# Performance work log

Hardware: AMD Instinct MI355X
Metric: run time of the kernel (lower is better)

The kernel has to match this reference:

```python
import jax, jax.numpy as jnp
import numpy as np

NUM_HEADS = 16
MASKED_BIAS = -10000.0


def setup_inputs() -> dict:
    key = jax.random.key(0)
    k1, k2, k3 = jax.random.split(key, 3)
    B, S, D = 4, 2048, 1024
    return {
        "hidden_states": jax.random.normal(k1, (B, S, D), dtype=jnp.float32),
        "attention_mask": jnp.ones((B, S), dtype=jnp.float32),
        "w_attn": jax.random.normal(k2, (D, 3 * D), dtype=jnp.float32) * 0.02,
        "b_attn": jax.random.normal(k3, (3 * D,), dtype=jnp.float32) * 0.1,
    }


def reference(hidden_states, attention_mask, w_attn, b_attn):
    B, S, D = hidden_states.shape
    H = NUM_HEADS
    Dh = D // H
    # Conv1D: x @ W + b  -> [B, S, 3D]
    qkv = hidden_states @ w_attn + b_attn
    q, k, v = jnp.split(qkv, 3, axis=-1)

    def split_heads(t):  # [B,S,D] -> [B,H,S,Dh]
        return t.reshape(B, S, H, Dh).transpose(0, 2, 1, 3)

    q, k, v = split_heads(q), split_heads(k), split_heads(v)
    present = jnp.stack([k, v], axis=0)  # concat_key_value

    # process_mask: (1 - mask) * -10000, broadcast [B,1,1,S]
    add_mask = (1.0 - attention_mask)[:, None, None, :] * MASKED_BIAS

    qk = jnp.einsum("bhqd,bhkd->bhqk", q, k)
    norm_qk = qk * (1.0 / float(Dh) ** 0.5)
    causal = jnp.tril(jnp.ones((S, S), dtype=bool))[None, None]
    attn_weights = jnp.where(causal, norm_qk, jnp.asarray(MASKED_BIAS, norm_qk.dtype))
    attn_weights = attn_weights + add_mask
    probs = jax.nn.softmax(attn_weights, axis=-1)
    attn_output = jnp.einsum("bhqk,bhkd->bhqd", probs, v)
    # merge heads -> [B,S,D]
    attn_output = attn_output.transpose(0, 2, 1, 3).reshape(B, S, D)
    return attn_output, present
```

## Files before the change

### kernel.cpp

```cpp
#include <hip/hip_runtime.h>
#include <stdint.h>


#define B_SZ    4
#define S_LEN   2048
#define D_MODEL 1024
#define N3      3072
#define H_NUM   16
#define DH      64
#define M_TOT   8192

typedef __attribute__((ext_vector_type(8))) short short8;
typedef __attribute__((ext_vector_type(4))) short bf16x4;
typedef __attribute__((ext_vector_type(4))) float f32x4;

#define LOG2E      1.4426950408889634f
#define SCL2E      0.18033688011112042f
#define MASKB2     (-14426.9504f)

__device__ __forceinline__ unsigned short f2b(float f) {
  union { float f; unsigned int u; } x;
  x.f = f;
  unsigned int u = x.u;
  u += 0x7fffu + ((u >> 16) & 1u);
  return (unsigned short)(u >> 16);
}

__device__ __forceinline__ unsigned int cvt_pk_bf16(float lo, float hi) {
  unsigned int r;
  asm("v_cvt_pk_bf16_f32 %0, %1, %2" : "=v"(r) : "v"(lo), "v"(hi));
  return r;
}

__device__ __forceinline__ float exp2_fast(float x) {
#if __has_builtin(__builtin_amdgcn_exp2f)
  return __builtin_amdgcn_exp2f(x);
#else
  return __expf(x * 0.6931471805599453f);
#endif
}

__device__ __forceinline__ f32x4 mfma16(bf16x4 a, bf16x4 b, f32x4 c) {
#if __has_builtin(__builtin_amdgcn_mfma_f32_16x16x16bf16_1k)
  return __builtin_amdgcn_mfma_f32_16x16x16bf16_1k(a, b, c, 0, 0, 0);
#else
  asm("v_mfma_f32_16x16x16_bf16 %0, %1, %2, %0" : "+v"(c) : "v"(a), "v"(b));
  return c;
#endif
}

__device__ __forceinline__ void async16(const void* g, void* l) {
  __builtin_amdgcn_global_load_lds((const __attribute__((address_space(1))) void*)g,
                                   (__attribute__((address_space(3))) void*)l,
                                   16, 0, 0);
}

__global__ void k_convert_x(const float* __restrict__ X, unsigned short* __restrict__ Xb) {
  const int i = (blockIdx.x * 256 + threadIdx.x) * 4;
  const float4 v = *(const float4*)(X + i);
  ushort4 o;
  o.x = f2b(v.x); o.y = f2b(v.y); o.z = f2b(v.z); o.w = f2b(v.w);
  *(ushort4*)(Xb + i) = o;
}

__global__ void k_wt(const float* __restrict__ W, unsigned short* __restrict__ Wt) {
  __shared__ float tile[32][33];
  const int n0 = blockIdx.x * 32, k0 = blockIdx.y * 32;
  const int tx = threadIdx.x, ty = threadIdx.y;
  for (int i = 0; i < 32; i += 8)
    tile[ty + i][tx] = W[(size_t)(k0 + ty + i) * N3 + n0 + tx];
  __syncthreads();
  for (int i = 0; i < 32; i += 8)
    Wt[(size_t)(n0 + ty + i) * D_MODEL + k0 + tx] = f2b(tile[tx][ty + i]);
}

__global__ __launch_bounds__(256) void k_gemm_qkv(
    const unsigned short* __restrict__ Xb, const unsigned short* __restrict__ Wt,
    const float* __restrict__ bias,
    unsigned short* __restrict__ Qb, unsigned short* __restrict__ Kb,
    float* __restrict__ presK, float* __restrict__ presV) {
  __shared__ __align__(16) unsigned short As[128 * 32];
  __shared__ __align__(16) unsigned short Bs[128 * 32];
  const int t = threadIdx.x;
  const int lane = t & 63, wave = t >> 6;
  const int g = lane >> 4, c = lane & 15;
  const int m0 = blockIdx.y * 128, n0 = blockIdx.x * 128;
  const int wm = (wave >> 1) * 64, wn = (wave & 1) * 64;

  const f32x4 zero = {0.f, 0.f, 0.f, 0.f};
  f32x4 acc[4][4];
  for (int i = 0; i < 4; ++i)
    for (int j = 0; j < 4; ++j) acc[i][j] = zero;

  const int row_a = t >> 2;
  const int col_a = (t & 3) * 8;
  const unsigned short* gA = Xb + (size_t)(m0 + row_a) * D_MODEL + col_a;
  const unsigned short* gB = Wt + (size_t)(n0 + row_a) * D_MODEL + col_a;
  const int wbase = wave * 1024;

  for (int k0 = 0; k0 < D_MODEL; k0 += 32) {
    __syncthreads();
    async16(gA + k0,                (char*)As + wbase);
    async16(gA + k0 + 64 * D_MODEL, (char*)As + 4096 + wbase);
    async16(gB + k0,                (char*)Bs + wbase);
    async16(gB + k0 + 64 * D_MODEL, (char*)Bs + 4096 + wbase);
    __syncthreads();

    short8 af[4], bf[4];
    for (int mi = 0; mi < 4; ++mi)
      af[mi] = *(const short8*)(As + (wm + mi * 16 + c) * 32 + g * 8);
    for (int ni = 0; ni < 4; ++ni)
      bf[ni] = *(const short8*)(Bs + (wn + ni * 16 + c) * 32 + g * 8);
    for (int mi = 0; mi < 4; ++mi)
      for (int ni = 0; ni < 4; ++ni)
        acc[mi][ni] = __builtin_amdgcn_mfma_f32_16x16x32_bf16(af[mi], bf[ni], acc[mi][ni], 0, 0, 0);
  }

  for (int ni = 0; ni < 4; ++ni) {
    const int n = n0 + wn + ni * 16 + c;
    const float bv = bias[n];
    const int sec = n >> 10;
    const int d = n & 1023;
    const int h = d >> 6, dh = d & 63;
    for (int mi = 0; mi < 4; ++mi) {
      for (int r = 0; r < 4; ++r) {
        const int m = m0 + wm + mi * 16 + g * 4 + r;
        const int b = m >> 11, s = m & 2047;
        const float val = acc[mi][ni][r] + bv;
        const size_t hidx = ((size_t)((b * H_NUM + h) * S_LEN + s)) * DH + dh;
        if (sec == 0) {
          Qb[hidx] = f2b(val);
        } else if (sec == 1) {
          presK[hidx] = val;
          Kb[hidx] = f2b(val);
        } else {
          presV[hidx] = val;
        }
      }
    }
  }
}

__global__ __launch_bounds__(256) void k_vt(const float* __restrict__ presV,
                                            unsigned short* __restrict__ Vt) {
  __shared__ unsigned short tile[64 * 72];
  const int t = threadIdx.x;
  const int bh = blockIdx.y;
  const int s0 = blockIdx.x * 64;
  const int row = t >> 2;
  const int dh0 = (t & 3) * 16;
  const float* src = presV + ((size_t)bh * S_LEN + s0 + row) * DH + dh0;
  for (int i = 0; i < 4; ++i) {
    const float4 v = *(const float4*)(src + i * 4);
    const int dh = dh0 + i * 4;
    tile[(dh + 0) * 72 + row] = f2b(v.x);
    tile[(dh + 1) * 72 + row] = f2b(v.y);
    tile[(dh + 2) * 72 + row] = f2b(v.z);
    tile[(dh + 3) * 72 + row] = f2b(v.w);
  }
  __syncthreads();
  const int dh = t >> 2, sc0 = (t & 3) * 16;
  unsigned short* dst = Vt + ((size_t)bh * DH + dh) * S_LEN + s0 + sc0;
  short8 o0, o1;
  for (int i = 0; i < 8; ++i) {
    o0[i] = (short)tile[dh * 72 + sc0 + i];
    o1[i] = (short)tile[dh * 72 + sc0 + 8 + i];
  }
  *(short8*)(dst) = o0;
  *(short8*)(dst + 8) = o1;
}

__global__ __launch_bounds__(512) void k_flash(
    const unsigned short* __restrict__ Qb, const unsigned short* __restrict__ Kb,
    const unsigned short* __restrict__ Vt, const float* __restrict__ mask,
    float* __restrict__ out) {
  __shared__ __align__(16) unsigned short Ks[2][64 * 64];
  __shared__ __align__(16) unsigned short Vs[2][64 * 64];
  __shared__ __align__(16) float Ams[S_LEN];
  const int t = threadIdx.x;
  const int lane = t & 63, wave = t >> 6;
  const int g = lane >> 4, c = lane & 15;
  const int bh = blockIdx.y;
  const int b = bh >> 4, h = bh & 15;
  const int srow = t >> 3;
  const int schunk = (t & 7) ^ (srow & 7);
  const unsigned short* gK0 = Kb + ((size_t)bh * S_LEN + srow) * DH + schunk * 8;
  const unsigned short* gV0 = Vt + ((size_t)bh * DH + srow) * S_LEN + schunk * 8;
  const int kslot = c & 7;

  {
    const float4 mv = *(const float4*)(mask + (size_t)b * S_LEN + t * 4);
    float4 o;
    o.x = (1.0f - mv.x) * MASKB2;
    o.y = (1.0f - mv.y) * MASKB2;
    o.z = (1.0f - mv.z) * MASKB2;
    o.w = (1.0f - mv.w) * MASKB2;
    *(float4*)(Ams + t * 4) = o;
  }

  const f32x4 zero = {0.f, 0.f, 0.f, 0.f};

  for (int phase = 0; phase < 2; ++phase) {
    const int x = phase ? 15 - (int)blockIdx.x : (int)blockIdx.x;
    const int qb = x * 128;
    const int qw = qb + wave * 16;
    const int qrow = qw + c;

    short8 bq[2];
    const size_t qoff = ((size_t)bh * S_LEN + qw) * DH;
#pragma unroll
    for (int kc = 0; kc < 2; ++kc)
      bq[kc] = *(const short8*)(Qb + qoff + (size_t)c * DH + kc * 32 + g * 8);

    float m_i = -1e30f, l_i = 0.f;
    f32x4 o_acc[4];
#pragma unroll
    for (int dt = 0; dt < 4; ++dt) o_acc[dt] = zero;

    const int nt = (qb + 128) >> 6;
    async16(gK0, (char*)(&Ks[0][0]) + wave * 1024);
    async16(gV0, (char*)(&Vs[0][0]) + wave * 1024);

    for (int tt = 0; tt < nt; ++tt) {
      const int kb = tt << 6;
      const int cur = tt & 1;
      if (tt + 1 < nt) {
        async16(gK0 + (size_t)(kb + 64) * DH, (char*)(&Ks[cur ^ 1][0]) + wave * 1024);
        async16(gV0 + (kb + 64),              (char*)(&Vs[cur ^ 1][0]) + wave * 1024);
        asm volatile("s_waitcnt vmcnt(2) lgkmcnt(0)" ::: "memory");
      } else {
        asm volatile("s_waitcnt vmcnt(0) lgkmcnt(0)" ::: "memory");
      }
      __builtin_amdgcn_s_barrier();
      __builtin_amdgcn_sched_barrier(0);

      if (qw + 16 > kb) {
        const unsigned short* ks_base = &Ks[cur][0];
        const unsigned short* vs_base = &Vs[cur][0];

        f32x4 sc[4];
#pragma unroll
        for (int ks = 0; ks < 4; ++ks) {
          f32x4 a = zero;
          const int krow = ks * 16 + c;
#pragma unroll
          for (int kc = 0; kc < 2; ++kc) {
            const short8 ak = *(const short8*)(ks_base + krow * 64 + (((kc * 4 + g) ^ kslot) * 8));
            a = __builtin_amdgcn_mfma_f32_16x16x32_bf16(ak, bq[kc], a, 0, 0, 0);
          }
          sc[ks] = a;
        }

        const bool need_causal = (kb + 63 > qw);
        float mxk[4];
#pragma unroll
        for (int ks = 0; ks < 4; ++ks) {
          const float4 amv = *(const float4*)(Ams + kb + ks * 16 + g * 4);
          float am4[4];
          am4[0] = amv.x; am4[1] = amv.y; am4[2] = amv.z; am4[3] = amv.w;
#pragma unroll
          for (int r = 0; r < 4; ++r) {
            float v = sc[ks][r] * SCL2E + am4[r];
            if (need_causal && (kb + ks * 16 + g * 4 + r > qrow))
              v = MASKB2 + am4[r];
            sc[ks][r] = v;
          }
          mxk[ks] = fmaxf(fmaxf(sc[ks][0], sc[ks][1]), fmaxf(sc[ks][2], sc[ks][3]));
        }

        float mx = fmaxf(fmaxf(mxk[0], mxk[1]), fmaxf(mxk[2], mxk[3]));
        mx = fmaxf(mx, __shfl_xor(mx, 16));
        mx = fmaxf(mx, __shfl_xor(mx, 32));
        const float mnew = fmaxf(m_i, mx);
        const float alpha = exp2_fast(m_i - mnew);
        m_i = mnew;

        bf16x4 pk[4];
        float rsk[4];
#pragma unroll
        for (int ks = 0; ks < 4; ++ks) {
          const float p0 = exp2_fast(sc[ks][0] - mnew);
          const float p1 = exp2_fast(sc[ks][1] - mnew);
          const float p2 = exp2_fast(sc[ks][2] - mnew);
          const float p3 = exp2_fast(sc[ks][3] - mnew);
          rsk[ks] = (p0 + p1) + (p2 + p3);
          union { unsigned int u[2]; bf16x4 v4; } pu;
          pu.u[0] = cvt_pk_bf16(p0, p1);
          pu.u[1] = cvt_pk_bf16(p2, p3);
          pk[ks] = pu.v4;
        }
        float rs = (rsk[0] + rsk[1]) + (rsk[2] + rsk[3]);
        rs += __shfl_xor(rs, 16);
        rs += __shfl_xor(rs, 32);
        l_i = l_i * alpha + rs;
#pragma unroll
        for (int dt = 0; dt < 4; ++dt) o_acc[dt] *= alpha;

#pragma unroll
        for (int dt = 0; dt < 4; ++dt) {
          const int vrow = dt * 16 + c;
#pragma unroll
          for (int ks = 0; ks < 4; ++ks) {
            const bf16x4 av = *(const bf16x4*)(vs_base + vrow * 64 +
                (((2 * ks + (g >> 1)) ^ kslot) * 8) + (g & 1) * 4);
            o_acc[dt] = mfma16(av, pk[ks], o_acc[dt]);
          }
        }
      }
      __builtin_amdgcn_sched_barrier(0);
      __builtin_amdgcn_s_barrier();
    }

    const float inv = 1.0f / l_i;
    float* orow = out + ((size_t)(b * S_LEN + qrow)) * D_MODEL + h * DH;
#pragma unroll
    for (int dt = 0; dt < 4; ++dt) {
      float4 o;
      o.x = o_acc[dt][0] * inv;
      o.y = o_acc[dt][1] * inv;
      o.z = o_acc[dt][2] * inv;
      o.w = o_acc[dt][3] * inv;
      *(float4*)(orow + dt * 16 + g * 4) = o;
    }
  }
}

extern "C" void kernel_launch(void* const* d_in, const int* in_sizes, int n_in,
                              void* d_out, int out_size, void* d_ws, size_t ws_size,
                              hipStream_t stream) {
  const float* X    = (const float*)d_in[0];
  const float* mask = (const float*)d_in[1];
  const float* W    = (const float*)d_in[2];
  const float* bias = (const float*)d_in[3];

  float* out   = (float*)d_out;
  float* presK = out + (size_t)M_TOT * D_MODEL;
  float* presV = presK + (size_t)M_TOT * D_MODEL;

  char* ws = (char*)d_ws;
  unsigned short* Xb = (unsigned short*)(ws);
  unsigned short* Wt = (unsigned short*)(ws + 16777216);
  unsigned short* Qb = (unsigned short*)(ws + 23068672);
  unsigned short* Kb = (unsigned short*)(ws + 39845888);
  unsigned short* Vt = (unsigned short*)(ws + 56623104);

  k_convert_x<<<dim3(8192), dim3(256), 0, stream>>>(X, Xb);
  k_wt<<<dim3(96, 32), dim3(32, 8), 0, stream>>>(W, Wt);
  k_gemm_qkv<<<dim3(24, 64), dim3(256), 0, stream>>>(Xb, Wt, bias, Qb, Kb, presK, presV);
  k_vt<<<dim3(32, 64), dim3(256), 0, stream>>>(presV, Vt);
  k_flash<<<dim3(8, 64), dim3(512), 0, stream>>>(Qb, Kb, Vt, mask, out);
}
```

Before: 306.8 us.

## Double-buffer QKV GEMM LDS loads with XOR swizzle and block remap

Turns the QKV projection GEMM's single-buffered LDS staging into a two-stage double buffer: async global-to-LDS copies for the next K slice are issued before the MFMAs on the current slice, with vmcnt waits and barriers in between. The LDS chunk layout is XOR-swizzled to reduce bank conflicts on the short8 fragment reads. Blocks are remapped from a flattened index so neighbouring workgroups share tiles in L2, and Q/K outputs use nontemporal stores. The cost is twice the LDS per block and hand-placed waitcnt and barrier ordering, which could lower occupancy or break if the async copy count assumptions are off.

```diff
diff --git a/kernel.cpp b/kernel.cpp
--- a/kernel.cpp
+++ b/kernel.cpp
@@ -79,12 +79,14 @@
     const float* __restrict__ bias,
     unsigned short* __restrict__ Qb, unsigned short* __restrict__ Kb,
     float* __restrict__ presK, float* __restrict__ presV) {
-  __shared__ __align__(16) unsigned short As[128 * 32];
-  __shared__ __align__(16) unsigned short Bs[128 * 32];
+  __shared__ __align__(16) unsigned short As[2][128 * 32];
+  __shared__ __align__(16) unsigned short Bs[2][128 * 32];
   const int t = threadIdx.x;
   const int lane = t & 63, wave = t >> 6;
   const int g = lane >> 4, c = lane & 15;
-  const int m0 = blockIdx.y * 128, n0 = blockIdx.x * 128;
+  const int flat = blockIdx.y * 24 + blockIdx.x;
+  const int nf = (flat & 7) * 192 + (flat >> 3);
+  const int n0 = (nf % 24) * 128, m0 = (nf / 24) * 128;
   const int wm = (wave >> 1) * 64, wn = (wave & 1) * 64;
 
   const f32x4 zero = {0.f, 0.f, 0.f, 0.f};
@@ -93,33 +95,53 @@
     for (int j = 0; j < 4; ++j) acc[i][j] = zero;
 
   const int row_a = t >> 2;
-  const int col_a = (t & 3) * 8;
-  const unsigned short* gA = Xb + (size_t)(m0 + row_a) * D_MODEL + col_a;
-  const unsigned short* gB = Wt + (size_t)(n0 + row_a) * D_MODEL + col_a;
+  const int schunk = ((t & 3) ^ (row_a & 3)) * 8;
+  const unsigned short* gA = Xb + (size_t)(m0 + row_a) * D_MODEL + schunk;
+  const unsigned short* gB = Wt + (size_t)(n0 + row_a) * D_MODEL + schunk;
   const int wbase = wave * 1024;
-
-  for (int k0 = 0; k0 < D_MODEL; k0 += 32) {
-    __syncthreads();
-    async16(gA + k0,                (char*)As + wbase);
-    async16(gA + k0 + 64 * D_MODEL, (char*)As + 4096 + wbase);
-    async16(gB + k0,                (char*)Bs + wbase);
-    async16(gB + k0 + 64 * D_MODEL, (char*)Bs + 4096 + wbase);
-    __syncthreads();
+  const int sw = (g ^ (c & 3)) * 8;
+
+  async16(gA,                (char*)As[0] + wbase);
+  async16(gA + 64 * D_MODEL, (char*)As[0] + 4096 + wbase);
+  async16(gB,                (char*)Bs[0] + wbase);
+  async16(gB + 64 * D_MODEL, (char*)Bs[0] + 4096 + wbase);
+
+  for (int it = 0; it < 32; ++it) {
+    const int cur = it & 1;
+    const int k0 = it * 32;
+    if (it < 31) {
+      async16(gA + k0 + 32,                (char*)As[cur ^ 1] + wbase);
+      async16(gA + k0 + 32 + 64 * D_MODEL, (char*)As[cur ^ 1] + 4096 + wbase);
+      async16(gB + k0 + 32,                (char*)Bs[cur ^ 1] + wbase);
+      async16(gB + k0 + 32 + 64 * D_MODEL, (char*)Bs[cur ^ 1] + 4096 + wbase);
+      asm volatile("s_waitcnt vmcnt(4)" ::: "memory");
+    } else {
+      asm volatile("s_waitcnt vmcnt(0)" ::: "memory");
+    }
+    __builtin_amdgcn_s_barrier();
+    __builtin_amdgcn_sched_barrier(0);
 
     short8 af[4], bf[4];
+#pragma unroll
     for (int mi = 0; mi < 4; ++mi)
-      af[mi] = *(const short8*)(As + (wm + mi * 16 + c) * 32 + g * 8);
+      af[mi] = *(const short8*)(&As[cur][0] + (wm + mi * 16 + c) * 32 + sw);
+#pragma unroll
     for (int ni = 0; ni < 4; ++ni)
-      bf[ni] = *(const short8*)(Bs + (wn + ni * 16 + c) * 32 + g * 8);
+      bf[ni] = *(const short8*)(&Bs[cur][0] + (wn + ni * 16 + c) * 32 + sw);
+#pragma unroll
     for (int mi = 0; mi < 4; ++mi)
+#pragma unroll
       for (int ni = 0; ni < 4; ++ni)
         acc[mi][ni] = __builtin_amdgcn_mfma_f32_16x16x32_bf16(af[mi], bf[ni], acc[mi][ni], 0, 0, 0);
-  }
-
+
+    __builtin_amdgcn_sched_barrier(0);
+    __builtin_amdgcn_s_barrier();
+  }
+
+  const int sec = n0 >> 10;
   for (int ni = 0; ni < 4; ++ni) {
     const int n = n0 + wn + ni * 16 + c;
     const float bv = bias[n];
-    const int sec = n >> 10;
     const int d = n & 1023;
     const int h = d >> 6, dh = d & 63;
     for (int mi = 0; mi < 4; ++mi) {
@@ -129,10 +151,10 @@
         const float val = acc[mi][ni][r] + bv;
         const size_t hidx = ((size_t)((b * H_NUM + h) * S_LEN + s)) * DH + dh;
         if (sec == 0) {
-          Qb[hidx] = f2b(val);
+          __builtin_nontemporal_store(f2b(val), &Qb[hidx]);
         } else if (sec == 1) {
-          presK[hidx] = val;
-          Kb[hidx] = f2b(val);
+          __builtin_nontemporal_store(val, &presK[hidx]);
+          __builtin_nontemporal_store(f2b(val), &Kb[hidx]);
         } else {
           presV[hidx] = val;
         }
```

Result: slower. 328.9 us (+7.2%).
